# Kernel tuning notes

Hardware: AMD Instinct MI355X
Metric: run time of the kernel (lower is better)

## Reference

```python
import jax, jax.numpy as jnp
import numpy as np

NEG = -9e15
ALPHA = 0.2  # leaky-relu slope


def gat_layer(h, mask, W, a, concat):
    # h: [N, Fin], W: [Fin, Fout], a: [2*Fout, 1], mask: [N, N]
    Wh = h @ W                                   # [N, Fout]
    F = Wh.shape[1]
    e = jax.nn.leaky_relu(Wh @ a[:F] + (Wh @ a[F:]).T, ALPHA)  # [N, N]
    att = jax.nn.softmax(jnp.where(mask > 0, e, NEG), axis=1)
    out = att @ Wh                               # [N, Fout]
    return jax.nn.elu(out) if concat else out


def gat(x, mask, W, a, Wo, ao):
    # W: [H, Fin, Fhid], a: [H, 2*Fhid, 1]
    heads = jax.vmap(lambda Wi, ai: gat_layer(x, mask, Wi, ai, True))(W, a)  # [H, N, Fhid]
    h = jnp.transpose(heads, (1, 0, 2)).reshape(x.shape[0], -1)  # [N, H*Fhid] (concat dim=1)
    return jax.nn.elu(gat_layer(h, mask, Wo, ao, False))


def setup_inputs() -> dict:
    key = jax.random.key(0)
    ks = jax.random.split(key, 16)
    N, Fin, H, Fhid, Ffin, P = 4096, 256, 4, 64, 64, 16
    x = jax.random.normal(ks[0], (N, Fin), jnp.float32)
    eye = jnp.eye(N, dtype=jnp.float32)
    sadj = jnp.maximum((jax.random.uniform(ks[1], (N, N)) < 0.005).astype(jnp.float32), eye)
    sadj2 = jnp.maximum((jax.random.uniform(ks[2], (N, N)) < 0.005).astype(jnp.float32), eye)
    s = 0.1
    inp = {
        "x": x, "sadj": sadj, "sadj2": sadj2,
        "W1": s * jax.random.normal(ks[3], (H, Fin, Fhid), jnp.float32),
        "a1": s * jax.random.normal(ks[4], (H, 2 * Fhid, 1), jnp.float32),
        "Wo1": s * jax.random.normal(ks[5], (H * Fhid, Ffin), jnp.float32),
        "ao1": s * jax.random.normal(ks[6], (2 * Ffin, 1), jnp.float32),
        "W2": s * jax.random.normal(ks[7], (H, Fin, Fhid), jnp.float32),
        "a2": s * jax.random.normal(ks[8], (H, 2 * Fhid, 1), jnp.float32),
        "Wo2": s * jax.random.normal(ks[9], (H * Fhid, Ffin), jnp.float32),
        "ao2": s * jax.random.normal(ks[10], (2 * Ffin, 1), jnp.float32),
        "Wp1": s * jax.random.normal(ks[11], (Ffin, P), jnp.float32),
        "bp1": jnp.zeros((P,), jnp.float32),
        "Wp2": s * jax.random.normal(ks[12], (P, 1), jnp.float32),
    }
    return inp


def reference(x, sadj, sadj2, W1, a1, Wo1, ao1, W2, a2, Wo2, ao2, Wp1, bp1, Wp2):
    emb1 = gat(x, sadj, W1, a1, Wo1, ao1)    # [N, Ffin]
    emb2 = gat(x, sadj2, W2, a2, Wo2, ao2)   # [N, Ffin]
    emb = jnp.stack([emb1, emb2], axis=1)    # [N, 2, Ffin]
    w = jnp.tanh(emb @ Wp1 + bp1) @ Wp2      # [N, 2, 1]
    beta = jax.nn.softmax(w, axis=1)
    return jnp.sum(beta * emb, axis=1)       # [N, Ffin]
```

## Files before the change

### kernel.cpp

```cpp
#include <hip/hip_runtime.h>
#include <hip/hip_bf16.h>
#include <stdint.h>


typedef short short8 __attribute__((ext_vector_type(8)));
typedef __bf16 bf16x8 __attribute__((ext_vector_type(8)));
typedef float floatx4 __attribute__((ext_vector_type(4)));
typedef unsigned int uintx4 __attribute__((ext_vector_type(4)));

#define MAXDEG 128
#define LRELU 0.2f

template <typename V>
__device__ inline auto mfma_impl(V a, V b, floatx4 c, int)
    -> decltype(__builtin_amdgcn_mfma_f32_16x16x32_bf16(a, b, c, 0, 0, 0)) {
  return __builtin_amdgcn_mfma_f32_16x16x32_bf16(a, b, c, 0, 0, 0);
}
template <typename V>
__device__ inline floatx4 mfma_impl(V a, V b, floatx4 c, long) {
  return __builtin_amdgcn_mfma_f32_16x16x32_bf16(
      __builtin_bit_cast(bf16x8, a), __builtin_bit_cast(bf16x8, b), c, 0, 0, 0);
}
__device__ inline floatx4 MFMA16(short8 a, short8 b, floatx4 c) {
  return mfma_impl(a, b, c, 0);
}

__device__ inline bool is_bf16_inputs(const void* sadj) {
  return ((*(const uint32_t*)sadj) & 0xFFFFu) == 0x3F80u;
}
__device__ inline float ldval(const void* p, size_t i, bool isbf) {
  if (isbf) return __bfloat162float(((const __hip_bfloat16*)p)[i]);
  return ((const float*)p)[i];
}
__device__ inline uint16_t f2bf_bits(float f) {
  __hip_bfloat16 h = __float2bfloat16(f);
  return *(uint16_t*)&h;
}
__device__ inline float bf2f(uint16_t u) {
  uint32_t i = ((uint32_t)u) << 16;
  return __builtin_bit_cast(float, i);
}

static constexpr size_t OFF_ADJ = 0;
static constexpr size_t OFF_DEG = OFF_ADJ + (size_t)2 * 4096 * MAXDEG * 4;
static constexpr size_t OFF_XB  = OFF_DEG + (size_t)2 * 4096 * 4;
static constexpr size_t OFF_WT  = OFF_XB  + (size_t)4096 * 256 * 2;
static constexpr size_t OFF_WOT = OFF_WT  + (size_t)2 * 4 * 64 * 256 * 2;
static constexpr size_t OFF_AV  = OFF_WOT + (size_t)2 * 64 * 256 * 2;
static constexpr size_t OFF_AOV = OFF_AV  + (size_t)2 * 4 * 128 * 4;
static constexpr size_t OFF_WP1 = OFF_AOV + (size_t)2 * 128 * 4;
static constexpr size_t OFF_BP1 = OFF_WP1 + (size_t)64 * 16 * 4;
static constexpr size_t OFF_WP2 = OFF_BP1 + 64;
static constexpr size_t OFF_WH1B = OFF_WP2 + 192;
static constexpr size_t OFF_S1  = OFF_WH1B + (size_t)2 * 4096 * 256 * 2;
static constexpr size_t OFF_D1  = OFF_S1  + (size_t)2 * 4 * 4096 * 4;
static constexpr size_t OFF_H2  = OFF_D1  + (size_t)2 * 4 * 4096 * 4;
static constexpr size_t OFF_WH2B = OFF_H2 + (size_t)2 * 4096 * 256 * 2;
static constexpr size_t OFF_S2  = OFF_WH2B + (size_t)2 * 4096 * 64 * 2;
static constexpr size_t OFF_D2  = OFF_S2  + (size_t)2 * 4096 * 4;

__device__ inline void adj_row(const uint16_t* mrow_bf, const float* mrow_f32,
                               bool isbf, int gn, int* adj, int* deg) {
  __shared__ int wtot[4];
  int t = threadIdx.x;
  uint32_t bits = 0;
  if (isbf) {
    uintx4 v0 = *((const uintx4*)mrow_bf + 2 * t);
    uintx4 v1 = *((const uintx4*)mrow_bf + 2 * t + 1);
    uint32_t wd[8] = {v0.x, v0.y, v0.z, v0.w, v1.x, v1.y, v1.z, v1.w};
#pragma unroll
    for (int k = 0; k < 16; ++k) {
      uint16_t val = (uint16_t)(wd[k >> 1] >> ((k & 1) * 16));
      if (val != 0 && !(val & 0x8000)) bits |= 1u << k;
    }
  } else {
#pragma unroll
    for (int j = 0; j < 4; ++j) {
      floatx4 v = *((const floatx4*)mrow_f32 + 4 * t + j);
      if (v.x > 0.f) bits |= 1u << (4 * j + 0);
      if (v.y > 0.f) bits |= 1u << (4 * j + 1);
      if (v.z > 0.f) bits |= 1u << (4 * j + 2);
      if (v.w > 0.f) bits |= 1u << (4 * j + 3);
    }
  }
  int c = __popc(bits);
  int lane = t & 63, wid = t >> 6;
  int pre = c;
#pragma unroll
  for (int o = 1; o < 64; o <<= 1) {
    int tv = __shfl_up(pre, o);
    if (lane >= o) pre += tv;
  }
  if (lane == 63) wtot[wid] = pre;
  __syncthreads();
  int base = 0, total = 0;
#pragma unroll
  for (int wq = 0; wq < 4; ++wq) {
    int v = wtot[wq];
    if (wq < wid) base += v;
    total += v;
  }
  int off = base + pre - c;
  int colbase = t * 16;
  int* out = adj + (size_t)gn * MAXDEG;
  while (bits) {
    int i = __ffs(bits) - 1;
    bits &= bits - 1;
    if (off < MAXDEG) out[off] = colbase + i;
    ++off;
  }
  if (t == 0) deg[gn] = total < MAXDEG ? total : MAXDEG;
}

__global__ __launch_bounds__(256) void k_pre_adj(
    const void* sadj, const void* sadj2, const void* x,
    const void* W1, const void* W2, const void* Wo1, const void* Wo2,
    const void* a1, const void* a2, const void* ao1, const void* ao2,
    const void* wp1, const void* bp1, const void* wp2,
    int* adj, int* deg, uint16_t* xb, uint16_t* Wt, uint16_t* Wot,
    float* Av, float* Aov, float* Wp1v, float* Bp1v, float* Wp2v) {
  bool isbf = is_bf16_inputs(sadj);
  int bid = blockIdx.x;
  if (bid < 8192) {
    int g = bid >> 12, n = bid & 4095;
    const void* mask = g ? sadj2 : sadj;
    adj_row((const uint16_t*)mask + (size_t)n * 4096,
            (const float*)mask + (size_t)n * 4096, isbf, bid, adj, deg);
    return;
  }
  if (bid < 9216) {
    int i0 = ((bid - 8192) * 256 + threadIdx.x) * 4;
    if (isbf) {
      *(uint64_t*)(xb + i0) = *(const uint64_t*)((const uint16_t*)x + i0);
    } else {
      const float* xf = (const float*)x;
      float4 f = *(const float4*)(xf + i0);
      xb[i0 + 0] = f2bf_bits(f.x);
      xb[i0 + 1] = f2bf_bits(f.y);
      xb[i0 + 2] = f2bf_bits(f.z);
      xb[i0 + 3] = f2bf_bits(f.w);
    }
    return;
  }
  int idx = (bid - 9216) * 256 + threadIdx.x;
  if (idx < 131072) {
    int k = idx & 255, f = (idx >> 8) & 63, h = (idx >> 14) & 3, g = idx >> 16;
    const void* W = g ? W2 : W1;
    Wt[idx] = f2bf_bits(ldval(W, (size_t)h * 16384 + (size_t)k * 64 + f, isbf));
  } else if (idx < 163840) {
    int j = idx - 131072;
    int k = j & 255, f = (j >> 8) & 63, g = j >> 14;
    const void* W = g ? Wo2 : Wo1;
    Wot[j] = f2bf_bits(ldval(W, (size_t)k * 64 + f, isbf));
  } else if (idx < 166176) {
    int q = idx - 163840;
    if (q < 512)        Av[q] = ldval(a1, q, isbf);
    else if (q < 1024)  Av[q] = ldval(a2, q - 512, isbf);
    else if (q < 1152)  Aov[q - 1024] = ldval(ao1, q - 1024, isbf);
    else if (q < 1280)  Aov[q - 1152 + 128] = ldval(ao2, q - 1152, isbf);
    else if (q < 2304)  Wp1v[q - 1280] = ldval(wp1, q - 1280, isbf);
    else if (q < 2320)  Bp1v[q - 2304] = ldval(bp1, q - 2304, isbf);
    else                Wp2v[q - 2320] = ldval(wp2, q - 2320, isbf);
  }
}

__global__ __launch_bounds__(256) void k_gemm1(const uint16_t* xb, const uint16_t* Wt,
                                               const float* Av,
                                               uint16_t* Wh1b, float* s1, float* d1) {
  int w = blockIdx.x * 4 + (threadIdx.x >> 6);
  int lane = threadIdx.x & 63;
  int q = lane >> 4, c = lane & 15;
  int g = w >> 10, rem = w & 1023;
  int m0 = (rem >> 2) << 4, h = rem & 3;
  const uint16_t* B = Wt + (size_t)(g * 4 + h) * 64 * 256;
  floatx4 acc[4] = {};
  const uint16_t* arow = xb + (size_t)(m0 + c) * 256 + q * 8;
  for (int kk = 0; kk < 8; ++kk) {
    short8 a = *(const short8*)(arow + kk * 32);
#pragma unroll
    for (int t = 0; t < 4; ++t) {
      short8 b = *(const short8*)(B + (size_t)(t * 16 + c) * 256 + kk * 32 + q * 8);
      acc[t] = MFMA16(a, b, acc[t]);
    }
  }
  uint16_t* Crow = Wh1b + (size_t)(g * 4096 + m0) * 256 + h * 64;
#pragma unroll
  for (int t = 0; t < 4; ++t)
#pragma unroll
    for (int r = 0; r < 4; ++r)
      Crow[(size_t)(q * 4 + r) * 256 + t * 16 + c] = f2bf_bits(acc[t][r]);
  const float* ag = Av + (g * 4 + h) * 128;
  float as[4], ad[4];
#pragma unroll
  for (int t = 0; t < 4; ++t) { as[t] = ag[t * 16 + c]; ad[t] = ag[64 + t * 16 + c]; }
#pragma unroll
  for (int r = 0; r < 4; ++r) {
    float ps = 0.f, pd = 0.f;
#pragma unroll
    for (int t = 0; t < 4; ++t) { ps += acc[t][r] * as[t]; pd += acc[t][r] * ad[t]; }
#pragma unroll
    for (int o = 1; o < 16; o <<= 1) { ps += __shfl_xor(ps, o); pd += __shfl_xor(pd, o); }
    if (c == 0) {
      int n = m0 + q * 4 + r;
      s1[((size_t)(g * 4096 + n)) * 4 + h] = ps;
      d1[((size_t)(g * 4096 + n)) * 4 + h] = pd;
    }
  }
}

__global__ __launch_bounds__(256) void k_att1(const int* adj, const int* deg,
    const float* s1, const float* d1, const uint16_t* Wh1b, uint16_t* h2) {
  __shared__ float pbuf[4][4][MAXDEG];
  __shared__ int jbuf[4][MAXDEG];
  int wv = threadIdx.x >> 6, lane = threadIdx.x & 63;
  int w = blockIdx.x * 4 + wv;
  int g = w >> 12;
  int gn = w;
  int dg = deg[gn];
  const int* nbr = adj + (size_t)gn * MAXDEG;
  float4 s4 = *(const float4*)(s1 + (size_t)gn * 4);
  const float4* d4 = (const float4*)(d1) + (size_t)g * 4096;

  bool v0 = lane < dg, v1 = lane + 64 < dg;
  int j0 = 0, j1 = 0;
  if (v0) j0 = nbr[lane];
  if (v1) j1 = nbr[lane + 64];
  float4 dj0 = d4[j0];
  float4 dj1 = d4[j1];
  if (v0) jbuf[wv][lane] = j0;
  if (v1) jbuf[wv][lane + 64] = j1;

  const float ninf = -3.0e38f;
  float sa[4] = {s4.x, s4.y, s4.z, s4.w};
  float d0a[4] = {dj0.x, dj0.y, dj0.z, dj0.w};
  float d1a[4] = {dj1.x, dj1.y, dj1.z, dj1.w};
#pragma unroll
  for (int h = 0; h < 4; ++h) {
    float t0 = sa[h] + d0a[h]; t0 = t0 > 0.f ? t0 : LRELU * t0;
    float t1 = sa[h] + d1a[h]; t1 = t1 > 0.f ? t1 : LRELU * t1;
    float e0 = v0 ? t0 : ninf;
    float e1 = v1 ? t1 : ninf;
    float m = fmaxf(e0, e1);
#pragma unroll
    for (int o = 32; o; o >>= 1) m = fmaxf(m, __shfl_xor(m, o));
    float p0 = v0 ? __expf(e0 - m) : 0.f;
    float p1 = v1 ? __expf(e1 - m) : 0.f;
    float l = p0 + p1;
#pragma unroll
    for (int o = 32; o; o >>= 1) l += __shfl_xor(l, o);
    float inv = __frcp_rn(l);
    pbuf[wv][h][lane] = p0 * inv;
    pbuf[wv][h][lane + 64] = p1 * inv;
  }
  int myh = lane >> 4;
  const float* prow = pbuf[wv][myh];
  const int* jb = jbuf[wv];
  const uint16_t* Wg = Wh1b + (size_t)g * 4096 * 256;
  float ax = 0.f, ay = 0.f, az = 0.f, aw = 0.f;
  for (int i = 0; i < dg; i += 8) {
    float pv[8];
    ushort4 wv8[8];
#pragma unroll
    for (int k = 0; k < 8; ++k) {
      int idx = i + k;
      bool vv = idx < dg;
      int sidx = vv ? idx : 0;
      int j = jb[sidx];
      pv[k] = vv ? prow[sidx] : 0.f;
      wv8[k] = *(const ushort4*)(Wg + (size_t)j * 256 + lane * 4);
    }
#pragma unroll
    for (int k = 0; k < 8; ++k) {
      ax += pv[k] * bf2f(wv8[k].x);
      ay += pv[k] * bf2f(wv8[k].y);
      az += pv[k] * bf2f(wv8[k].z);
      aw += pv[k] * bf2f(wv8[k].w);
    }
  }
  ax = ax > 0.f ? ax : __expf(ax) - 1.f;
  ay = ay > 0.f ? ay : __expf(ay) - 1.f;
  az = az > 0.f ? az : __expf(az) - 1.f;
  aw = aw > 0.f ? aw : __expf(aw) - 1.f;
  ushort4 o4 = {f2bf_bits(ax), f2bf_bits(ay), f2bf_bits(az), f2bf_bits(aw)};
  *(ushort4*)(h2 + (size_t)gn * 256 + lane * 4) = o4;
}

__global__ __launch_bounds__(256) void k_gemm2(const uint16_t* h2, const uint16_t* Wot,
                                               const float* Aov,
                                               uint16_t* Wh2b, float* s2, float* d2) {
  int w = blockIdx.x * 4 + (threadIdx.x >> 6);
  int lane = threadIdx.x & 63;
  int q = lane >> 4, c = lane & 15;
  int g = w >> 8, m0 = (w & 255) << 4;
  const uint16_t* A = h2 + (size_t)g * 4096 * 256;
  const uint16_t* B = Wot + (size_t)g * 64 * 256;
  floatx4 acc[4] = {};
  const uint16_t* arow = A + (size_t)(m0 + c) * 256 + q * 8;
  for (int kk = 0; kk < 8; ++kk) {
    short8 a = *(const short8*)(arow + kk * 32);
#pragma unroll
    for (int t = 0; t < 4; ++t) {
      short8 b = *(const short8*)(B + (size_t)(t * 16 + c) * 256 + kk * 32 + q * 8);
      acc[t] = MFMA16(a, b, acc[t]);
    }
  }
  uint16_t* Crow = Wh2b + (size_t)(g * 4096 + m0) * 64;
#pragma unroll
  for (int t = 0; t < 4; ++t)
#pragma unroll
    for (int r = 0; r < 4; ++r)
      Crow[(size_t)(q * 4 + r) * 64 + t * 16 + c] = f2bf_bits(acc[t][r]);
  const float* ag = Aov + g * 128;
  float as[4], ad[4];
#pragma unroll
  for (int t = 0; t < 4; ++t) { as[t] = ag[t * 16 + c]; ad[t] = ag[64 + t * 16 + c]; }
#pragma unroll
  for (int r = 0; r < 4; ++r) {
    float ps = 0.f, pd = 0.f;
#pragma unroll
    for (int t = 0; t < 4; ++t) { ps += acc[t][r] * as[t]; pd += acc[t][r] * ad[t]; }
#pragma unroll
    for (int o = 1; o < 16; o <<= 1) { ps += __shfl_xor(ps, o); pd += __shfl_xor(pd, o); }
    if (c == 0) {
      int n = m0 + q * 4 + r;
      s2[g * 4096 + n] = ps;
      d2[g * 4096 + n] = pd;
    }
  }
}

__global__ __launch_bounds__(256) void k_att2f(const int* adj, const int* deg,
    const float* s2, const float* d2, const uint16_t* Wh2b,
    const float* Wp1v, const float* Bp1v, const float* Wp2v,
    const void* sadj, void* out) {
  __shared__ float pbuf[4][MAXDEG];
  __shared__ int jbuf[4][MAXDEG];
  __shared__ float emb_s[4][64];
  __shared__ float st_s[2][32];
  __shared__ float sw_s[2][2];
  int wv = threadIdx.x >> 6, lane = threadIdx.x & 63;
  int g = wv >> 1, nl = wv & 1;
  int n = blockIdx.x * 2 + nl;
  int gn = g * 4096 + n;
  int dg = deg[gn];
  const int* nbr = adj + (size_t)gn * MAXDEG;
  float sn = s2[gn];
  const float* dp = d2 + (size_t)g * 4096;

  bool v0 = lane < dg, v1 = lane + 64 < dg;
  int j0 = 0, j1 = 0;
  if (v0) j0 = nbr[lane];
  if (v1) j1 = nbr[lane + 64];
  float dd0 = dp[j0], dd1 = dp[j1];
  if (v0) jbuf[wv][lane] = j0;
  if (v1) jbuf[wv][lane + 64] = j1;

  const float ninf = -3.0e38f;
  float t0 = sn + dd0; t0 = t0 > 0.f ? t0 : LRELU * t0;
  float t1 = sn + dd1; t1 = t1 > 0.f ? t1 : LRELU * t1;
  float e0 = v0 ? t0 : ninf;
  float e1 = v1 ? t1 : ninf;
  float m = fmaxf(e0, e1);
#pragma unroll
  for (int o = 32; o; o >>= 1) m = fmaxf(m, __shfl_xor(m, o));
  float p0 = v0 ? __expf(e0 - m) : 0.f;
  float p1 = v1 ? __expf(e1 - m) : 0.f;
  float l = p0 + p1;
#pragma unroll
  for (int o = 32; o; o >>= 1) l += __shfl_xor(l, o);
  float inv = __frcp_rn(l);
  pbuf[wv][lane] = p0 * inv;
  pbuf[wv][lane + 64] = p1 * inv;

  int mye = lane >> 4, c4 = lane & 15;
  const uint16_t* Wg = Wh2b + (size_t)g * 4096 * 64;
  float ax = 0.f, ay = 0.f, az = 0.f, aw = 0.f;
  for (int i = 0; i < dg; i += 8) {
    int ia = i + mye, ib = i + 4 + mye;
    bool va = ia < dg, vb = ib < dg;
    int sa_ = va ? ia : 0, sb_ = vb ? ib : 0;
    int ja = jbuf[wv][sa_], jb2 = jbuf[wv][sb_];
    float pa = va ? pbuf[wv][sa_] : 0.f;
    float pb = vb ? pbuf[wv][sb_] : 0.f;
    ushort4 wa = *(const ushort4*)(Wg + (size_t)ja * 64 + c4 * 4);
    ushort4 wb = *(const ushort4*)(Wg + (size_t)jb2 * 64 + c4 * 4);
    ax += pa * bf2f(wa.x) + pb * bf2f(wb.x);
    ay += pa * bf2f(wa.y) + pb * bf2f(wb.y);
    az += pa * bf2f(wa.z) + pb * bf2f(wb.z);
    aw += pa * bf2f(wa.w) + pb * bf2f(wb.w);
  }
#pragma unroll
  for (int o = 16; o <= 32; o <<= 1) {
    ax += __shfl_xor(ax, o);
    ay += __shfl_xor(ay, o);
    az += __shfl_xor(az, o);
    aw += __shfl_xor(aw, o);
  }
  if (lane < 16) {
    ax = ax > 0.f ? ax : __expf(ax) - 1.f;
    ay = ay > 0.f ? ay : __expf(ay) - 1.f;
    az = az > 0.f ? az : __expf(az) - 1.f;
    aw = aw > 0.f ? aw : __expf(aw) - 1.f;
    float4 r = {ax, ay, az, aw};
    *(float4*)&emb_s[wv][c4 * 4] = r;
  }
  __syncthreads();
  if (wv < 2) {
    float e1v = emb_s[wv][lane];
    float e2v = emb_s[2 + wv][lane];
    if (lane < 32) {
      int gg = lane >> 4, p = lane & 15;
      float s = Bp1v[p];
      const float* eb = emb_s[gg * 2 + wv];
      for (int f = 0; f < 64; ++f) s += eb[f] * Wp1v[f * 16 + p];
      st_s[wv][lane] = tanhf(s);
    }
    if (lane < 2) {
      float s = 0.f;
      for (int p = 0; p < 16; ++p) s += st_s[wv][lane * 16 + p] * Wp2v[p];
      sw_s[wv][lane] = s;
    }
    float w0 = sw_s[wv][0], w1 = sw_s[wv][1];
    float mx = fmaxf(w0, w1);
    float q0 = __expf(w0 - mx), q1 = __expf(w1 - mx);
    float qi = 1.f / (q0 + q1);
    float v = (q0 * e1v + q1 * e2v) * qi;
    if (is_bf16_inputs(sadj)) ((uint16_t*)out)[(size_t)n * 64 + lane] = f2bf_bits(v);
    else ((float*)out)[(size_t)n * 64 + lane] = v;
  }
}

extern "C" void kernel_launch(void* const* d_in, const int* in_sizes, int n_in,
                              void* d_out, int out_size, void* d_ws, size_t ws_size,
                              hipStream_t stream) {
  const void* x    = d_in[0];
  const void* sadj = d_in[1];
  const void* sadj2 = d_in[2];
  const void* W1  = d_in[3];
  const void* a1  = d_in[4];
  const void* Wo1 = d_in[5];
  const void* ao1 = d_in[6];
  const void* W2  = d_in[7];
  const void* a2  = d_in[8];
  const void* Wo2 = d_in[9];
  const void* ao2 = d_in[10];
  const void* Wp1 = d_in[11];
  const void* bp1 = d_in[12];
  const void* Wp2 = d_in[13];

  char* ws = (char*)d_ws;
  int* adj      = (int*)(ws + OFF_ADJ);
  int* deg      = (int*)(ws + OFF_DEG);
  uint16_t* xb  = (uint16_t*)(ws + OFF_XB);
  uint16_t* Wt  = (uint16_t*)(ws + OFF_WT);
  uint16_t* Wot = (uint16_t*)(ws + OFF_WOT);
  float* Av     = (float*)(ws + OFF_AV);
  float* Aov    = (float*)(ws + OFF_AOV);
  float* Wp1v   = (float*)(ws + OFF_WP1);
  float* Bp1v   = (float*)(ws + OFF_BP1);
  float* Wp2v   = (float*)(ws + OFF_WP2);
  uint16_t* Wh1b = (uint16_t*)(ws + OFF_WH1B);
  float* s1     = (float*)(ws + OFF_S1);
  float* d1     = (float*)(ws + OFF_D1);
  uint16_t* h2  = (uint16_t*)(ws + OFF_H2);
  uint16_t* Wh2b = (uint16_t*)(ws + OFF_WH2B);
  float* s2     = (float*)(ws + OFF_S2);
  float* d2     = (float*)(ws + OFF_D2);

  k_pre_adj<<<9872, 256, 0, stream>>>(sadj, sadj2, x, W1, W2, Wo1, Wo2,
                                      a1, a2, ao1, ao2, Wp1, bp1, Wp2,
                                      adj, deg, xb, Wt, Wot,
                                      Av, Aov, Wp1v, Bp1v, Wp2v);
  k_gemm1<<<512, 256, 0, stream>>>(xb, Wt, Av, Wh1b, s1, d1);
  k_att1<<<2048, 256, 0, stream>>>(adj, deg, s1, d1, Wh1b, h2);
  k_gemm2<<<128, 256, 0, stream>>>(h2, Wot, Aov, Wh2b, s2, d2);
  k_att2f<<<2048, 256, 0, stream>>>(adj, deg, s2, d2, Wh2b,
                                    Wp1v, Bp1v, Wp2v, sadj, d_out);
}
```

Measured before the change: 218.4 us.

## Fuse all stages into one persistent cooperative kernel with grid syncs

Replaces the five separate kernel launches with one cooperative persistent kernel of 1024 blocks that runs each stage in grid-strided loops separated by grid.sync(). The input conversion now runs first, so the adjacency build and the first GEMM can share a phase. The aim is to remove per-launch overhead and the tail idle time between kernels. In exchange, grid-wide barriers cost something, occupancy is limited by the fixed grid, and if the cooperative launch fails the code falls back to separate launches.

```diff
diff --git a/kernel.cpp b/kernel.cpp
--- a/kernel.cpp
+++ b/kernel.cpp
@@ -1,6 +1,9 @@
 #include <hip/hip_runtime.h>
 #include <hip/hip_bf16.h>
+#include <hip/hip_cooperative_groups.h>
 #include <stdint.h>
+
+namespace cg = cooperative_groups;
 
 
 typedef short short8 __attribute__((ext_vector_type(8)));
@@ -10,6 +13,7 @@
 
 #define MAXDEG 128
 #define LRELU 0.2f
+#define SMEM_BYTES 10496
 
 template <typename V>
 __device__ inline auto mfma_impl(V a, V b, floatx4 c, int)
@@ -59,9 +63,63 @@
 static constexpr size_t OFF_S2  = OFF_WH2B + (size_t)2 * 4096 * 64 * 2;
 static constexpr size_t OFF_D2  = OFF_S2  + (size_t)2 * 4096 * 4;
 
-__device__ inline void adj_row(const uint16_t* mrow_bf, const float* mrow_f32,
-                               bool isbf, int gn, int* adj, int* deg) {
-  __shared__ int wtot[4];
+struct KArgs {
+  const void *x, *sadj, *sadj2, *W1, *a1, *Wo1, *ao1, *W2, *a2, *Wo2, *ao2,
+      *Wp1, *bp1, *Wp2;
+  int* adj;
+  int* deg;
+  uint16_t *xb, *Wt, *Wot;
+  float *Av, *Aov, *Wp1v, *Bp1v, *Wp2v;
+  uint16_t* Wh1b;
+  float *s1, *d1;
+  uint16_t *h2, *Wh2b;
+  float *s2, *d2;
+  void* out;
+};
+
+__device__ inline void dev_conv(int vb, bool isbf, const KArgs& A) {
+  if (vb < 1024) {
+    int i0 = (vb * 256 + threadIdx.x) * 4;
+    if (isbf) {
+      *(uint64_t*)(A.xb + i0) = *(const uint64_t*)((const uint16_t*)A.x + i0);
+    } else {
+      const float* xf = (const float*)A.x;
+      float4 f = *(const float4*)(xf + i0);
+      A.xb[i0 + 0] = f2bf_bits(f.x);
+      A.xb[i0 + 1] = f2bf_bits(f.y);
+      A.xb[i0 + 2] = f2bf_bits(f.z);
+      A.xb[i0 + 3] = f2bf_bits(f.w);
+    }
+    return;
+  }
+  int idx = (vb - 1024) * 256 + threadIdx.x;
+  if (idx < 131072) {
+    int k = idx & 255, f = (idx >> 8) & 63, h = (idx >> 14) & 3, g = idx >> 16;
+    const void* W = g ? A.W2 : A.W1;
+    A.Wt[idx] = f2bf_bits(ldval(W, (size_t)h * 16384 + (size_t)k * 64 + f, isbf));
+  } else if (idx < 163840) {
+    int j = idx - 131072;
+    int k = j & 255, f = (j >> 8) & 63, g = j >> 14;
+    const void* W = g ? A.Wo2 : A.Wo1;
+    A.Wot[j] = f2bf_bits(ldval(W, (size_t)k * 64 + f, isbf));
+  } else if (idx < 166176) {
+    int q = idx - 163840;
+    if (q < 512)        A.Av[q] = ldval(A.a1, q, isbf);
+    else if (q < 1024)  A.Av[q] = ldval(A.a2, q - 512, isbf);
+    else if (q < 1152)  A.Aov[q - 1024] = ldval(A.ao1, q - 1024, isbf);
+    else if (q < 1280)  A.Aov[q - 1152 + 128] = ldval(A.ao2, q - 1152, isbf);
+    else if (q < 2304)  A.Wp1v[q - 1280] = ldval(A.Wp1, q - 1280, isbf);
+    else if (q < 2320)  A.Bp1v[q - 2304] = ldval(A.bp1, q - 2304, isbf);
+    else                A.Wp2v[q - 2320] = ldval(A.Wp2, q - 2320, isbf);
+  }
+}
+
+__device__ inline void dev_adj_row(int gn, bool isbf, const KArgs& A, char* smem) {
+  int* wtot = (int*)smem;
+  int g = gn >> 12, n = gn & 4095;
+  const void* mask = g ? A.sadj2 : A.sadj;
+  const uint16_t* mrow_bf = (const uint16_t*)mask + (size_t)n * 4096;
+  const float* mrow_f32 = (const float*)mask + (size_t)n * 4096;
   int t = threadIdx.x;
   uint32_t bits = 0;
   if (isbf) {
@@ -102,79 +160,26 @@
   }
   int off = base + pre - c;
   int colbase = t * 16;
-  int* out = adj + (size_t)gn * MAXDEG;
+  int* out = A.adj + (size_t)gn * MAXDEG;
   while (bits) {
     int i = __ffs(bits) - 1;
     bits &= bits - 1;
     if (off < MAXDEG) out[off] = colbase + i;
     ++off;
   }
-  if (t == 0) deg[gn] = total < MAXDEG ? total : MAXDEG;
-}
-
-__global__ __launch_bounds__(256) void k_pre_adj(
-    const void* sadj, const void* sadj2, const void* x,
-    const void* W1, const void* W2, const void* Wo1, const void* Wo2,
-    const void* a1, const void* a2, const void* ao1, const void* ao2,
-    const void* wp1, const void* bp1, const void* wp2,
-    int* adj, int* deg, uint16_t* xb, uint16_t* Wt, uint16_t* Wot,
-    float* Av, float* Aov, float* Wp1v, float* Bp1v, float* Wp2v) {
-  bool isbf = is_bf16_inputs(sadj);
-  int bid = blockIdx.x;
-  if (bid < 8192) {
-    int g = bid >> 12, n = bid & 4095;
-    const void* mask = g ? sadj2 : sadj;
-    adj_row((const uint16_t*)mask + (size_t)n * 4096,
-            (const float*)mask + (size_t)n * 4096, isbf, bid, adj, deg);
-    return;
-  }
-  if (bid < 9216) {
-    int i0 = ((bid - 8192) * 256 + threadIdx.x) * 4;
-    if (isbf) {
-      *(uint64_t*)(xb + i0) = *(const uint64_t*)((const uint16_t*)x + i0);
-    } else {
-      const float* xf = (const float*)x;
-      float4 f = *(const float4*)(xf + i0);
-      xb[i0 + 0] = f2bf_bits(f.x);
-      xb[i0 + 1] = f2bf_bits(f.y);
-      xb[i0 + 2] = f2bf_bits(f.z);
-      xb[i0 + 3] = f2bf_bits(f.w);
-    }
-    return;
-  }
-  int idx = (bid - 9216) * 256 + threadIdx.x;
-  if (idx < 131072) {
-    int k = idx & 255, f = (idx >> 8) & 63, h = (idx >> 14) & 3, g = idx >> 16;
-    const void* W = g ? W2 : W1;
-    Wt[idx] = f2bf_bits(ldval(W, (size_t)h * 16384 + (size_t)k * 64 + f, isbf));
-  } else if (idx < 163840) {
-    int j = idx - 131072;
-    int k = j & 255, f = (j >> 8) & 63, g = j >> 14;
-    const void* W = g ? Wo2 : Wo1;
-    Wot[j] = f2bf_bits(ldval(W, (size_t)k * 64 + f, isbf));
-  } else if (idx < 166176) {
-    int q = idx - 163840;
-    if (q < 512)        Av[q] = ldval(a1, q, isbf);
-    else if (q < 1024)  Av[q] = ldval(a2, q - 512, isbf);
-    else if (q < 1152)  Aov[q - 1024] = ldval(ao1, q - 1024, isbf);
-    else if (q < 1280)  Aov[q - 1152 + 128] = ldval(ao2, q - 1152, isbf);
-    else if (q < 2304)  Wp1v[q - 1280] = ldval(wp1, q - 1280, isbf);
-    else if (q < 2320)  Bp1v[q - 2304] = ldval(bp1, q - 2304, isbf);
-    else                Wp2v[q - 2320] = ldval(wp2, q - 2320, isbf);
-  }
-}
-
-__global__ __launch_bounds__(256) void k_gemm1(const uint16_t* xb, const uint16_t* Wt,
-                                               const float* Av,
-                                               uint16_t* Wh1b, float* s1, float* d1) {
-  int w = blockIdx.x * 4 + (threadIdx.x >> 6);
+  if (t == 0) A.deg[gn] = total < MAXDEG ? total : MAXDEG;
+  __syncthreads();
+}
+
+__device__ inline void dev_gemm1(int vb, const KArgs& A) {
+  int w = vb * 4 + (threadIdx.x >> 6);
   int lane = threadIdx.x & 63;
   int q = lane >> 4, c = lane & 15;
   int g = w >> 10, rem = w & 1023;
   int m0 = (rem >> 2) << 4, h = rem & 3;
-  const uint16_t* B = Wt + (size_t)(g * 4 + h) * 64 * 256;
+  const uint16_t* B = A.Wt + (size_t)(g * 4 + h) * 64 * 256;
   floatx4 acc[4] = {};
-  const uint16_t* arow = xb + (size_t)(m0 + c) * 256 + q * 8;
+  const uint16_t* arow = A.xb + (size_t)(m0 + c) * 256 + q * 8;
   for (int kk = 0; kk < 8; ++kk) {
     short8 a = *(const short8*)(arow + kk * 32);
 #pragma unroll
@@ -183,13 +188,13 @@
       acc[t] = MFMA16(a, b, acc[t]);
     }
   }
-  uint16_t* Crow = Wh1b + (size_t)(g * 4096 + m0) * 256 + h * 64;
+  uint16_t* Crow = A.Wh1b + (size_t)(g * 4096 + m0) * 256 + h * 64;
 #pragma unroll
   for (int t = 0; t < 4; ++t)
 #pragma unroll
     for (int r = 0; r < 4; ++r)
       Crow[(size_t)(q * 4 + r) * 256 + t * 16 + c] = f2bf_bits(acc[t][r]);
-  const float* ag = Av + (g * 4 + h) * 128;
+  const float* ag = A.Av + (g * 4 + h) * 128;
   float as[4], ad[4];
 #pragma unroll
   for (int t = 0; t < 4; ++t) { as[t] = ag[t * 16 + c]; ad[t] = ag[64 + t * 16 + c]; }
@@ -202,24 +207,23 @@
     for (int o = 1; o < 16; o <<= 1) { ps += __shfl_xor(ps, o); pd += __shfl_xor(pd, o); }
     if (c == 0) {
       int n = m0 + q * 4 + r;
-      s1[((size_t)(g * 4096 + n)) * 4 + h] = ps;
-      d1[((size_t)(g * 4096 + n)) * 4 + h] = pd;
-    }
-  }
-}
-
-__global__ __launch_bounds__(256) void k_att1(const int* adj, const int* deg,
-    const float* s1, const float* d1, const uint16_t* Wh1b, uint16_t* h2) {
-  __shared__ float pbuf[4][4][MAXDEG];
-  __shared__ int jbuf[4][MAXDEG];
+      A.s1[((size_t)(g * 4096 + n)) * 4 + h] = ps;
+      A.d1[((size_t)(g * 4096 + n)) * 4 + h] = pd;
+    }
+  }
+}
+
+__device__ inline void dev_att1(int vb, const KArgs& A, char* smem) {
+  float* pbuf = (float*)smem;
+  int* jbuf = (int*)(smem + 8192);
   int wv = threadIdx.x >> 6, lane = threadIdx.x & 63;
-  int w = blockIdx.x * 4 + wv;
+  int w = vb * 4 + wv;
   int g = w >> 12;
   int gn = w;
-  int dg = deg[gn];
-  const int* nbr = adj + (size_t)gn * MAXDEG;
-  float4 s4 = *(const float4*)(s1 + (size_t)gn * 4);
-  const float4* d4 = (const float4*)(d1) + (size_t)g * 4096;
+  int dg = A.deg[gn];
+  const int* nbr = A.adj + (size_t)gn * MAXDEG;
+  float4 s4 = *(const float4*)(A.s1 + (size_t)gn * 4);
+  const float4* d4 = (const float4*)(A.d1) + (size_t)g * 4096;
 
   bool v0 = lane < dg, v1 = lane + 64 < dg;
   int j0 = 0, j1 = 0;
@@ -227,8 +231,8 @@
   if (v1) j1 = nbr[lane + 64];
   float4 dj0 = d4[j0];
   float4 dj1 = d4[j1];
-  if (v0) jbuf[wv][lane] = j0;
-  if (v1) jbuf[wv][lane + 64] = j1;
+  if (v0) jbuf[wv * 128 + lane] = j0;
+  if (v1) jbuf[wv * 128 + lane + 64] = j1;
 
   const float ninf = -3.0e38f;
   float sa[4] = {s4.x, s4.y, s4.z, s4.w};
@@ -249,13 +253,13 @@
 #pragma unroll
     for (int o = 32; o; o >>= 1) l += __shfl_xor(l, o);
     float inv = __frcp_rn(l);
-    pbuf[wv][h][lane] = p0 * inv;
-    pbuf[wv][h][lane + 64] = p1 * inv;
+    pbuf[(wv * 4 + h) * 128 + lane] = p0 * inv;
+    pbuf[(wv * 4 + h) * 128 + lane + 64] = p1 * inv;
   }
   int myh = lane >> 4;
-  const float* prow = pbuf[wv][myh];
-  const int* jb = jbuf[wv];
-  const uint16_t* Wg = Wh1b + (size_t)g * 4096 * 256;
+  const float* prow = pbuf + (wv * 4 + myh) * 128;
+  const int* jb = jbuf + wv * 128;
+  const uint16_t* Wg = A.Wh1b + (size_t)g * 4096 * 256;
   float ax = 0.f, ay = 0.f, az = 0.f, aw = 0.f;
   for (int i = 0; i < dg; i += 8) {
     float pv[8];
@@ -263,10 +267,10 @@
 #pragma unroll
     for (int k = 0; k < 8; ++k) {
       int idx = i + k;
-      bool vv = idx < dg;
-      int sidx = vv ? idx : 0;
+      bool vvk = idx < dg;
+      int sidx = vvk ? idx : 0;
       int j = jb[sidx];
-      pv[k] = vv ? prow[sidx] : 0.f;
+      pv[k] = vvk ? prow[sidx] : 0.f;
       wv8[k] = *(const ushort4*)(Wg + (size_t)j * 256 + lane * 4);
     }
 #pragma unroll
@@ -282,20 +286,18 @@
   az = az > 0.f ? az : __expf(az) - 1.f;
   aw = aw > 0.f ? aw : __expf(aw) - 1.f;
   ushort4 o4 = {f2bf_bits(ax), f2bf_bits(ay), f2bf_bits(az), f2bf_bits(aw)};
-  *(ushort4*)(h2 + (size_t)gn * 256 + lane * 4) = o4;
-}
-
-__global__ __launch_bounds__(256) void k_gemm2(const uint16_t* h2, const uint16_t* Wot,
-                                               const float* Aov,
-                                               uint16_t* Wh2b, float* s2, float* d2) {
-  int w = blockIdx.x * 4 + (threadIdx.x >> 6);
+  *(ushort4*)(A.h2 + (size_t)gn * 256 + lane * 4) = o4;
+}
+
+__device__ inline void dev_gemm2(int vb, const KArgs& A) {
+  int w = vb * 4 + (threadIdx.x >> 6);
   int lane = threadIdx.x & 63;
   int q = lane >> 4, c = lane & 15;
   int g = w >> 8, m0 = (w & 255) << 4;
-  const uint16_t* A = h2 + (size_t)g * 4096 * 256;
-  const uint16_t* B = Wot + (size_t)g * 64 * 256;
+  const uint16_t* Am = A.h2 + (size_t)g * 4096 * 256;
+  const uint16_t* B = A.Wot + (size_t)g * 64 * 256;
   floatx4 acc[4] = {};
-  const uint16_t* arow = A + (size_t)(m0 + c) * 256 + q * 8;
+  const uint16_t* arow = Am + (size_t)(m0 + c) * 256 + q * 8;
   for (int kk = 0; kk < 8; ++kk) {
     short8 a = *(const short8*)(arow + kk * 32);
 #pragma unroll
@@ -304,13 +306,13 @@
       acc[t] = MFMA16(a, b, acc[t]);
     }
   }
-  uint16_t* Crow = Wh2b + (size_t)(g * 4096 + m0) * 64;
+  uint16_t* Crow = A.Wh2b + (size_t)(g * 4096 + m0) * 64;
 #pragma unroll
   for (int t = 0; t < 4; ++t)
 #pragma unroll
     for (int r = 0; r < 4; ++r)
       Crow[(size_t)(q * 4 + r) * 64 + t * 16 + c] = f2bf_bits(acc[t][r]);
-  const float* ag = Aov + g * 128;
+  const float* ag = A.Aov + g * 128;
   float as[4], ad[4];
 #pragma unroll
   for (int t = 0; t < 4; ++t) { as[t] = ag[t * 16 + c]; ad[t] = ag[64 + t * 16 + c]; }
@@ -323,37 +325,34 @@
     for (int o = 1; o < 16; o <<= 1) { ps += __shfl_xor(ps, o); pd += __shfl_xor(pd, o); }
     if (c == 0) {
       int n = m0 + q * 4 + r;
-      s2[g * 4096 + n] = ps;
-      d2[g * 4096 + n] = pd;
-    }
-  }
-}
-
-__global__ __launch_bounds__(256) void k_att2f(const int* adj, const int* deg,
-    const float* s2, const float* d2, const uint16_t* Wh2b,
-    const float* Wp1v, const float* Bp1v, const float* Wp2v,
-    const void* sadj, void* out) {
-  __shared__ float pbuf[4][MAXDEG];
-  __shared__ int jbuf[4][MAXDEG];
-  __shared__ float emb_s[4][64];
-  __shared__ float st_s[2][32];
-  __shared__ float sw_s[2][2];
+      A.s2[g * 4096 + n] = ps;
+      A.d2[g * 4096 + n] = pd;
+    }
+  }
+}
+
+__device__ inline void dev_att2f(int vb, const KArgs& A, char* smem, bool isbf) {
+  float* pbuf = (float*)smem;
+  int* jbuf = (int*)(smem + 2048);
+  float* emb_s = (float*)(smem + 4096);
+  float* st_s = (float*)(smem + 5120);
+  float* sw_s = (float*)(smem + 5376);
   int wv = threadIdx.x >> 6, lane = threadIdx.x & 63;
   int g = wv >> 1, nl = wv & 1;
-  int n = blockIdx.x * 2 + nl;
+  int n = vb * 2 + nl;
   int gn = g * 4096 + n;
-  int dg = deg[gn];
-  const int* nbr = adj + (size_t)gn * MAXDEG;
-  float sn = s2[gn];
-  const float* dp = d2 + (size_t)g * 4096;
+  int dg = A.deg[gn];
+  const int* nbr = A.adj + (size_t)gn * MAXDEG;
+  float sn = A.s2[gn];
+  const float* dp = A.d2 + (size_t)g * 4096;
 
   bool v0 = lane < dg, v1 = lane + 64 < dg;
   int j0 = 0, j1 = 0;
   if (v0) j0 = nbr[lane];
   if (v1) j1 = nbr[lane + 64];
   float dd0 = dp[j0], dd1 = dp[j1];
-  if (v0) jbuf[wv][lane] = j0;
-  if (v1) jbuf[wv][lane + 64] = j1;
+  if (v0) jbuf[wv * 128 + lane] = j0;
+  if (v1) jbuf[wv * 128 + lane + 64] = j1;
 
   const float ninf = -3.0e38f;
   float t0 = sn + dd0; t0 = t0 > 0.f ? t0 : LRELU * t0;
@@ -369,19 +368,19 @@
 #pragma unroll
   for (int o = 32; o; o >>= 1) l += __shfl_xor(l, o);
   float inv = __frcp_rn(l);
-  pbuf[wv][lane] = p0 * inv;
-  pbuf[wv][lane + 64] = p1 * inv;
+  pbuf[wv * 128 + lane] = p0 * inv;
+  pbuf[wv * 128 + lane + 64] = p1 * inv;
 
   int mye = lane >> 4, c4 = lane & 15;
-  const uint16_t* Wg = Wh2b + (size_t)g * 4096 * 64;
+  const uint16_t* Wg = A.Wh2b + (size_t)g * 4096 * 64;
   float ax = 0.f, ay = 0.f, az = 0.f, aw = 0.f;
   for (int i = 0; i < dg; i += 8) {
     int ia = i + mye, ib = i + 4 + mye;
-    bool va = ia < dg, vb = ib < dg;
-    int sa_ = va ? ia : 0, sb_ = vb ? ib : 0;
-    int ja = jbuf[wv][sa_], jb2 = jbuf[wv][sb_];
-    float pa = va ? pbuf[wv][sa_] : 0.f;
-    float pb = vb ? pbuf[wv][sb_] : 0.f;
+    bool va = ia < dg, vb2 = ib < dg;
+    int sa_ = va ? ia : 0, sb_ = vb2 ? ib : 0;
+    int ja = jbuf[wv * 128 + sa_], jb2 = jbuf[wv * 128 + sb_];
+    float pa = va ? pbuf[wv * 128 + sa_] : 0.f;
+    float pb = vb2 ? pbuf[wv * 128 + sb_] : 0.f;
     ushort4 wa = *(const ushort4*)(Wg + (size_t)ja * 64 + c4 * 4);
     ushort4 wb = *(const ushort4*)(Wg + (size_t)jb2 * 64 + c4 * 4);
     ax += pa * bf2f(wa.x) + pb * bf2f(wb.x);
@@ -402,78 +401,107 @@
     az = az > 0.f ? az : __expf(az) - 1.f;
     aw = aw > 0.f ? aw : __expf(aw) - 1.f;
     float4 r = {ax, ay, az, aw};
-    *(float4*)&emb_s[wv][c4 * 4] = r;
+    *(float4*)&emb_s[wv * 64 + c4 * 4] = r;
   }
   __syncthreads();
   if (wv < 2) {
-    float e1v = emb_s[wv][lane];
-    float e2v = emb_s[2 + wv][lane];
+    float e1v = emb_s[wv * 64 + lane];
+    float e2v = emb_s[(2 + wv) * 64 + lane];
     if (lane < 32) {
       int gg = lane >> 4, p = lane & 15;
-      float s = Bp1v[p];
-      const float* eb = emb_s[gg * 2 + wv];
-      for (int f = 0; f < 64; ++f) s += eb[f] * Wp1v[f * 16 + p];
-      st_s[wv][lane] = tanhf(s);
+      float s = A.Bp1v[p];
+      const float* eb = emb_s + (gg * 2 + wv) * 64;
+      for (int f = 0; f < 64; ++f) s += eb[f] * A.Wp1v[f * 16 + p];
+      st_s[wv * 32 + lane] = tanhf(s);
     }
     if (lane < 2) {
       float s = 0.f;
-      for (int p = 0; p < 16; ++p) s += st_s[wv][lane * 16 + p] * Wp2v[p];
-      sw_s[wv][lane] = s;
-    }
-    float w0 = sw_s[wv][0], w1 = sw_s[wv][1];
+      for (int p = 0; p < 16; ++p) s += st_s[wv * 32 + lane * 16 + p] * A.Wp2v[p];
+      sw_s[wv * 2 + lane] = s;
+    }
+    float w0 = sw_s[wv * 2 + 0], w1 = sw_s[wv * 2 + 1];
     float mx = fmaxf(w0, w1);
     float q0 = __expf(w0 - mx), q1 = __expf(w1 - mx);
     float qi = 1.f / (q0 + q1);
     float v = (q0 * e1v + q1 * e2v) * qi;
-    if (is_bf16_inputs(sadj)) ((uint16_t*)out)[(size_t)n * 64 + lane] = f2bf_bits(v);
-    else ((float*)out)[(size_t)n * 64 + lane] = v;
-  }
+    if (isbf) ((uint16_t*)A.out)[(size_t)n * 64 + lane] = f2bf_bits(v);
+    else ((float*)A.out)[(size_t)n * 64 + lane] = v;
+  }
+  __syncthreads();
+}
+
+__global__ __launch_bounds__(256, 4) void k_all(KArgs A) {
+  cg::grid_group grid = cg::this_grid();
+  __shared__ __align__(16) char smem[SMEM_BYTES];
+  bool isbf = is_bf16_inputs(A.sadj);
+  for (int vb = blockIdx.x; vb < 1680; vb += gridDim.x) dev_conv(vb, isbf, A);
+  grid.sync();
+  for (int vb = blockIdx.x; vb < 8704; vb += gridDim.x) {
+    if (vb < 8192) dev_adj_row(vb, isbf, A, smem);
+    else dev_gemm1(vb - 8192, A);
+  }
+  grid.sync();
+  for (int vb = blockIdx.x; vb < 2048; vb += gridDim.x) dev_att1(vb, A, smem);
+  grid.sync();
+  for (int vb = blockIdx.x; vb < 128; vb += gridDim.x) dev_gemm2(vb, A);
+  grid.sync();
+  for (int vb = blockIdx.x; vb < 2048; vb += gridDim.x) dev_att2f(vb, A, smem, isbf);
+}
+
+__global__ __launch_bounds__(256) void kf_pre(KArgs A) {
+  __shared__ __align__(16) char smem[SMEM_BYTES];
+  bool isbf = is_bf16_inputs(A.sadj);
+  int bid = blockIdx.x;
+  if (bid < 8192) dev_adj_row(bid, isbf, A, smem);
+  else dev_conv(bid - 8192, isbf, A);
+}
+__global__ __launch_bounds__(256) void kf_gemm1(KArgs A) { dev_gemm1(blockIdx.x, A); }
+__global__ __launch_bounds__(256) void kf_att1(KArgs A) {
+  __shared__ __align__(16) char smem[SMEM_BYTES];
+  dev_att1(blockIdx.x, A, smem);
+}
+__global__ __launch_bounds__(256) void kf_gemm2(KArgs A) { dev_gemm2(blockIdx.x, A); }
+__global__ __launch_bounds__(256) void kf_att2f(KArgs A) {
+  __shared__ __align__(16) char smem[SMEM_BYTES];
+  dev_att2f(blockIdx.x, A, smem, is_bf16_inputs(A.sadj));
 }
 
 extern "C" void kernel_launch(void* const* d_in, const int* in_sizes, int n_in,
                               void* d_out, int out_size, void* d_ws, size_t ws_size,
                               hipStream_t stream) {
-  const void* x    = d_in[0];
-  const void* sadj = d_in[1];
-  const void* sadj2 = d_in[2];
-  const void* W1  = d_in[3];
-  const void* a1  = d_in[4];
-  const void* Wo1 = d_in[5];
-  const void* ao1 = d_in[6];
-  const void* W2  = d_in[7];
-  const void* a2  = d_in[8];
-  const void* Wo2 = d_in[9];
-  const void* ao2 = d_in[10];
-  const void* Wp1 = d_in[11];
-  const void* bp1 = d_in[12];
-  const void* Wp2 = d_in[13];
-
   char* ws = (char*)d_ws;
-  int* adj      = (int*)(ws + OFF_ADJ);
-  int* deg      = (int*)(ws + OFF_DEG);
-  uint16_t* xb  = (uint16_t*)(ws + OFF_XB);
-  uint16_t* Wt  = (uint16_t*)(ws + OFF_WT);
-  uint16_t* Wot = (uint16_t*)(ws + OFF_WOT);
-  float* Av     = (float*)(ws + OFF_AV);
-  float* Aov    = (float*)(ws + OFF_AOV);
-  float* Wp1v   = (float*)(ws + OFF_WP1);
-  float* Bp1v   = (float*)(ws + OFF_BP1);
-  float* Wp2v   = (float*)(ws + OFF_WP2);
-  uint16_t* Wh1b = (uint16_t*)(ws + OFF_WH1B);
-  float* s1     = (float*)(ws + OFF_S1);
-  float* d1     = (float*)(ws + OFF_D1);
-  uint16_t* h2  = (uint16_t*)(ws + OFF_H2);
-  uint16_t* Wh2b = (uint16_t*)(ws + OFF_WH2B);
-  float* s2     = (float*)(ws + OFF_S2);
-  float* d2     = (float*)(ws + OFF_D2);
-
-  k_pre_adj<<<9872, 256, 0, stream>>>(sadj, sadj2, x, W1, W2, Wo1, Wo2,
-                                      a1, a2, ao1, ao2, Wp1, bp1, Wp2,
-                                      adj, deg, xb, Wt, Wot,
-                                      Av, Aov, Wp1v, Bp1v, Wp2v);
-  k_gemm1<<<512, 256, 0, stream>>>(xb, Wt, Av, Wh1b, s1, d1);
-  k_att1<<<2048, 256, 0, stream>>>(adj, deg, s1, d1, Wh1b, h2);
-  k_gemm2<<<128, 256, 0, stream>>>(h2, Wot, Aov, Wh2b, s2, d2);
-  k_att2f<<<2048, 256, 0, stream>>>(adj, deg, s2, d2, Wh2b,
-                                    Wp1v, Bp1v, Wp2v, sadj, d_out);
-}
+  KArgs A;
+  A.x = d_in[0];  A.sadj = d_in[1]; A.sadj2 = d_in[2];
+  A.W1 = d_in[3]; A.a1 = d_in[4];  A.Wo1 = d_in[5]; A.ao1 = d_in[6];
+  A.W2 = d_in[7]; A.a2 = d_in[8];  A.Wo2 = d_in[9]; A.ao2 = d_in[10];
+  A.Wp1 = d_in[11]; A.bp1 = d_in[12]; A.Wp2 = d_in[13];
+  A.adj = (int*)(ws + OFF_ADJ);
+  A.deg = (int*)(ws + OFF_DEG);
+  A.xb = (uint16_t*)(ws + OFF_XB);
+  A.Wt = (uint16_t*)(ws + OFF_WT);
+  A.Wot = (uint16_t*)(ws + OFF_WOT);
+  A.Av = (float*)(ws + OFF_AV);
+  A.Aov = (float*)(ws + OFF_AOV);
+  A.Wp1v = (float*)(ws + OFF_WP1);
+  A.Bp1v = (float*)(ws + OFF_BP1);
+  A.Wp2v = (float*)(ws + OFF_WP2);
+  A.Wh1b = (uint16_t*)(ws + OFF_WH1B);
+  A.s1 = (float*)(ws + OFF_S1);
+  A.d1 = (float*)(ws + OFF_D1);
+  A.h2 = (uint16_t*)(ws + OFF_H2);
+  A.Wh2b = (uint16_t*)(ws + OFF_WH2B);
+  A.s2 = (float*)(ws + OFF_S2);
+  A.d2 = (float*)(ws + OFF_D2);
+  A.out = d_out;
+
+  void* params[] = {&A};
+  hipError_t e = hipLaunchCooperativeKernel((const void*)k_all, dim3(1024),
+                                            dim3(256), params, 0, stream);
+  if (e != hipSuccess) {
+    kf_pre<<<9872, 256, 0, stream>>>(A);
+    kf_gemm1<<<512, 256, 0, stream>>>(A);
+    kf_att1<<<2048, 256, 0, stream>>>(A);
+    kf_gemm2<<<128, 256, 0, stream>>>(A);
+    kf_att2f<<<2048, 256, 0, stream>>>(A);
+  }
+}
```

New measurement: 693.4 us. 3.18x slower.
